# Optimization experiments

Hardware: AMD Instinct MI355X
Metric: run time of the kernel (lower is better)

The kernel has to match this reference:

```python
import jax, jax.numpy as jnp
import numpy as np

B, L, T = 4096, 4096, 2


def setup_inputs() -> dict:
    key = jax.random.key(0)
    k1, k2, k3, k4, k5 = jax.random.split(key, 5)
    emissions = jax.random.normal(k1, (B, L, T), dtype=jnp.float32)
    tags = jax.random.randint(k2, (B, L), 0, T, dtype=jnp.int64)
    mask = jnp.ones((B, L), dtype=jnp.bool_)
    # learned CRF parameters, init uniform(-0.1, 0.1) as in the module
    transitions = jax.random.uniform(k3, (T, T), jnp.float32, -0.1, 0.1)
    start_transitions = jax.random.uniform(k4, (T,), jnp.float32, -0.1, 0.1)
    end_transitions = jax.random.uniform(k5, (T,), jnp.float32, -0.1, 0.1)
    return {"emissions": emissions, "tags": tags, "mask": mask,
            "transitions": transitions, "start_transitions": start_transitions,
            "end_transitions": end_transitions}


def _gold_score(emissions, tags, mask, transitions, start_transitions, end_transitions):
    maskf = mask.astype(emissions.dtype)
    # t=0 contribution
    score = start_transitions[tags[:, 0]] + jnp.take_along_axis(
        emissions[:, 0], tags[:, 0:1], axis=1)[:, 0]
    # steps 1..L-1, fully vectorized
    emit = jnp.take_along_axis(emissions, tags[:, :, None], axis=2)[:, :, 0]  # [B,L]
    trans = transitions[tags[:, 1:], tags[:, :-1]]                            # [B,L-1]
    score = score + jnp.sum((emit[:, 1:] + trans) * maskf[:, 1:], axis=1)
    # end transition from last valid tag
    last_idx = (jnp.sum(mask.astype(jnp.int32), axis=1) - 1)[:, None]         # [B,1]
    last_tags = jnp.take_along_axis(tags, last_idx.astype(tags.dtype), axis=1)[:, 0]
    return score + end_transitions[last_tags]


def _normalizer(emissions, mask, transitions, start_transitions, end_transitions):
    alpha0 = start_transitions + emissions[:, 0]  # [B,T]

    def step(alpha, xm):
        emit, m = xm  # emit: [B,T], m: [B]
        # scores[b, cur, prev] = alpha[b, prev] + transitions[cur, prev]
        scores = alpha[:, None, :] + transitions[None, :, :]
        alpha_new = jax.nn.logsumexp(scores, axis=2) + emit
        alpha = jnp.where(m[:, None], alpha_new, alpha)
        return alpha, None

    emits = jnp.swapaxes(emissions[:, 1:], 0, 1)  # [L-1,B,T]
    masks = jnp.swapaxes(mask[:, 1:], 0, 1)       # [L-1,B]
    alpha, _ = jax.lax.scan(step, alpha0, (emits, masks))
    return jax.nn.logsumexp(alpha + end_transitions, axis=1)  # [B]


def reference(emissions, tags, mask, transitions, start_transitions, end_transitions):
    gold = _gold_score(emissions, tags, mask, transitions, start_transitions, end_transitions)
    fwd = _normalizer(emissions, mask, transitions, start_transitions, end_transitions)
    seq_lengths = jnp.clip(jnp.sum(mask, axis=1).astype(emissions.dtype), 1.0)
    nll = (fwd - gold) / seq_lengths
    return jnp.mean(nll)
```

## Files before the change

kernel.cpp:

```cpp
#include <hip/hip_runtime.h>


typedef float f32x4 __attribute__((ext_vector_type(4)));
typedef int   i32x4 __attribute__((ext_vector_type(4)));

__global__ __launch_bounds__(256, 4) void crf_rows(
    const float* __restrict__ em,
    const int*   __restrict__ tags,
    const float* __restrict__ tr,
    const float* __restrict__ st,
    const float* __restrict__ en,
    float* __restrict__ rows,
    int L)
{
    const int b    = blockIdx.x;
    const int tid  = threadIdx.x;
    const int lane = tid & 63;
    const int wid  = tid >> 6;

    const float t00 = tr[0], t01 = tr[1], t10 = tr[2], t11 = tr[3];
    const float s0 = st[0], s1 = st[1];
    const float en0 = en[0], en1 = en[1];
    const float T00 = __expf(t00), T01 = __expf(t01);
    const float T10 = __expf(t10), T11 = __expf(t11);

    const float* erow = em + (size_t)b * (size_t)(2 * L);
    const int*   trow = tags + (size_t)b * (size_t)L;
    const int l0 = tid << 4;

    f32x4 ev[8];
    const f32x4* ep = reinterpret_cast<const f32x4*>(erow + 2 * l0);
#pragma unroll
    for (int i = 0; i < 8; ++i) ev[i] = ep[i];
    i32x4 tv[4];
    const i32x4* tp = reinterpret_cast<const i32x4*>(trow + l0);
#pragma unroll
    for (int i = 0; i < 2; ++i) tv[i] = tp[i];
    tv[2] = tp[2]; tv[3] = tp[3];
    int pv = trow[tid ? (l0 - 1) : 0];
    asm volatile("" ::
        "v"(ev[0]), "v"(ev[1]), "v"(ev[2]), "v"(ev[3]),
        "v"(ev[4]), "v"(ev[5]), "v"(ev[6]), "v"(ev[7]),
        "v"(tv[0]), "v"(tv[1]), "v"(tv[2]), "v"(tv[3]), "v"(pv));

    const bool is0 = (tid == 0);
    int prev = is0 ? 0 : pv;

    float Q00 = 1.f, Q01 = 0.f, Q10 = 0.f, Q11 = 1.f;
    float ls = 0.f;
    float gold = 0.f;

#pragma unroll
    for (int k = 0; k < 16; ++k) {
        const f32x4 v = ev[k >> 1];
        const float e0 = (k & 1) ? v.z : v.x;
        const float e1 = (k & 1) ? v.w : v.y;
        const i32x4 t4 = tv[k >> 2];
        const int cur = ((k & 3) == 0) ? t4.x : ((k & 3) == 1) ? t4.y
                      : ((k & 3) == 2) ? t4.z : t4.w;

        const float R = __expf(e1 - e0);
        if (!(k == 0 && is0)) {
            const float n00 = fmaf(T00, Q00, T01 * Q10);
            const float n01 = fmaf(T00, Q01, T01 * Q11);
            const float n10 = R * fmaf(T10, Q00, T11 * Q10);
            const float n11 = R * fmaf(T10, Q01, T11 * Q11);
            Q00 = n00; Q01 = n01; Q10 = n10; Q11 = n11;
            ls += e0;
        }

        const float ee  = cur ? e1 : e0;
        const float trv = cur ? (prev ? t11 : t10) : (prev ? t01 : t00);
        if (k == 0 && is0) {
            gold += (cur ? s1 : s0) + ee;
        } else {
            gold += ee + trv;
        }
        prev = cur;
    }
    if (tid == 255) gold += prev ? en1 : en0;

    {
        const float m = fmaxf(fmaxf(Q00, Q01), fmaxf(Q10, Q11));
        const float inv = __builtin_amdgcn_rcpf(m);
        ls += __logf(m);
        Q00 *= inv; Q01 *= inv; Q10 *= inv; Q11 *= inv;
    }
    float sv = ls;

#pragma unroll
    for (int d = 1; d < 64; d <<= 1) {
        const float qb00 = __shfl_down(Q00, d);
        const float qb01 = __shfl_down(Q01, d);
        const float qb10 = __shfl_down(Q10, d);
        const float qb11 = __shfl_down(Q11, d);
        const float sb   = __shfl_down(sv, d);
        const float gb   = __shfl_down(gold, d);
        if (lane + d < 64) {
            const float c00 = fmaf(qb00, Q00, qb01 * Q10);
            const float c01 = fmaf(qb00, Q01, qb01 * Q11);
            const float c10 = fmaf(qb10, Q00, qb11 * Q10);
            const float c11 = fmaf(qb10, Q01, qb11 * Q11);
            Q00 = c00; Q01 = c01; Q10 = c10; Q11 = c11;
            sv += sb; gold += gb;
        }
        if (d == 2 || d == 8 || d == 32) {
            const float m = fmaxf(fmaxf(Q00, Q01), fmaxf(Q10, Q11));
            const float inv = __builtin_amdgcn_rcpf(m);
            sv += __logf(m);
            Q00 *= inv; Q01 *= inv; Q10 *= inv; Q11 *= inv;
        }
    }

    __shared__ float sh[4][6];
    if (lane == 0) {
        sh[wid][0] = sv;  sh[wid][1] = Q00; sh[wid][2] = Q01;
        sh[wid][3] = Q10; sh[wid][4] = Q11; sh[wid][5] = gold;
    }
    __syncthreads();

    if (tid == 0) {
        float S = sh[0][0];
        float A00 = sh[0][1], A01 = sh[0][2], A10 = sh[0][3], A11 = sh[0][4];
        float g = sh[0][5];
#pragma unroll
        for (int w = 1; w < 4; ++w) {
            const float b00 = sh[w][1], b01 = sh[w][2], b10 = sh[w][3], b11 = sh[w][4];
            const float c00 = fmaf(b00, A00, b01 * A10);
            const float c01 = fmaf(b00, A01, b01 * A11);
            const float c10 = fmaf(b10, A00, b11 * A10);
            const float c11 = fmaf(b10, A01, b11 * A11);
            A00 = c00; A01 = c01; A10 = c10; A11 = c11;
            S += sh[w][0]; g += sh[w][5];
        }
        const float a0 = s0 + erow[0];
        const float a1 = s1 + erow[1];
        const float am = fmaxf(a0, a1);
        const float x0 = __expf(a0 - am);
        const float x1 = __expf(a1 - am);
        const float w0 = fmaf(A00, x0, A01 * x1);
        const float w1 = fmaf(A10, x0, A11 * x1);
        const float z  = fmaxf(fmaf(__expf(en0), w0, __expf(en1) * w1), 1e-37f);
        const float fwd = S + am + __logf(z);
        rows[b] = (fwd - g) * (1.0f / (float)L);
    }
}

__global__ __launch_bounds__(256) void reduce_mean(
    const float* __restrict__ rows, float* __restrict__ out, int n)
{
    float s = 0.f;
    for (int i = threadIdx.x; i < n; i += 256) s += rows[i];
#pragma unroll
    for (int sft = 32; sft >= 1; sft >>= 1) s += __shfl_down(s, sft);
    __shared__ float sh[4];
    if ((threadIdx.x & 63) == 0) sh[threadIdx.x >> 6] = s;
    __syncthreads();
    if (threadIdx.x == 0) {
        out[0] = (sh[0] + sh[1] + sh[2] + sh[3]) / (float)n;
    }
}

extern "C" void kernel_launch(void* const* d_in, const int* in_sizes, int n_in,
                              void* d_out, int out_size, void* d_ws, size_t ws_size,
                              hipStream_t stream) {
    const float* em   = (const float*)d_in[0];
    const int*   tags = (const int*)d_in[1];
    const float* tr = (const float*)d_in[3];
    const float* st = (const float*)d_in[4];
    const float* en = (const float*)d_in[5];

    const int B = 4096, L = 4096;
    float* rows = (float*)d_ws;

    crf_rows<<<B, 256, 0, stream>>>(em, tags, tr, st, en, rows, L);
    reduce_mean<<<1, 256, 0, stream>>>(rows, (float*)d_out, B);
}
```

Before: 39.96 us.

## Issue raw asm loads, overlap forward pass with tag loads, count transitions algebraically

Replaces the compiler-generated loads with inline-asm global_load_dwordx4 and uses a partial vmcnt wait, so the forward matrix-product loop runs on emissions while the tag loads are still in flight. The gold score is rebuilt from integer counts of transition types times the four transition values, which removes the per-step selects. Occupancy hint goes from 4 to 6, one renormalisation is dropped from the shuffle tree, and thread 0 reuses register emissions instead of reloading from global memory. The risks are register pressure at the higher occupancy, the fragility of manual waitcnt handling, and wider floating-point range between renormalisations.

```diff
diff --git a/kernel.cpp b/kernel.cpp
--- a/kernel.cpp
+++ b/kernel.cpp
@@ -4,7 +4,7 @@
 typedef float f32x4 __attribute__((ext_vector_type(4)));
 typedef int   i32x4 __attribute__((ext_vector_type(4)));
 
-__global__ __launch_bounds__(256, 4) void crf_rows(
+__global__ __launch_bounds__(256, 6) void crf_rows(
     const float* __restrict__ em,
     const int*   __restrict__ tags,
     const float* __restrict__ tr,
@@ -21,6 +21,9 @@
     const float t00 = tr[0], t01 = tr[1], t10 = tr[2], t11 = tr[3];
     const float s0 = st[0], s1 = st[1];
     const float en0 = en[0], en1 = en[1];
+    asm volatile("" :: "v"(t00), "v"(t01), "v"(t10), "v"(t11),
+                       "v"(s0), "v"(s1), "v"(en0), "v"(en1));
+
     const float T00 = __expf(t00), T01 = __expf(t01);
     const float T10 = __expf(t10), T11 = __expf(t11);
 
@@ -28,28 +31,56 @@
     const int*   trow = tags + (size_t)b * (size_t)L;
     const int l0 = tid << 4;
 
+    unsigned long long ea = (unsigned long long)(erow + 2 * l0);
+    unsigned long long ta = (unsigned long long)(trow + l0);
+    unsigned long long pa = (unsigned long long)(trow + (tid ? (l0 - 1) : 0));
+
     f32x4 ev[8];
-    const f32x4* ep = reinterpret_cast<const f32x4*>(erow + 2 * l0);
-#pragma unroll
-    for (int i = 0; i < 8; ++i) ev[i] = ep[i];
     i32x4 tv[4];
-    const i32x4* tp = reinterpret_cast<const i32x4*>(trow + l0);
-#pragma unroll
-    for (int i = 0; i < 2; ++i) tv[i] = tp[i];
-    tv[2] = tp[2]; tv[3] = tp[3];
-    int pv = trow[tid ? (l0 - 1) : 0];
-    asm volatile("" ::
-        "v"(ev[0]), "v"(ev[1]), "v"(ev[2]), "v"(ev[3]),
-        "v"(ev[4]), "v"(ev[5]), "v"(ev[6]), "v"(ev[7]),
-        "v"(tv[0]), "v"(tv[1]), "v"(tv[2]), "v"(tv[3]), "v"(pv));
+    int pv;
+    asm volatile("global_load_dwordx4 %0, %1, off"            : "=v"(ev[0]) : "v"(ea));
+    asm volatile("global_load_dwordx4 %0, %1, off offset:16"  : "=v"(ev[1]) : "v"(ea));
+    asm volatile("global_load_dwordx4 %0, %1, off offset:32"  : "=v"(ev[2]) : "v"(ea));
+    asm volatile("global_load_dwordx4 %0, %1, off offset:48"  : "=v"(ev[3]) : "v"(ea));
+    asm volatile("global_load_dwordx4 %0, %1, off offset:64"  : "=v"(ev[4]) : "v"(ea));
+    asm volatile("global_load_dwordx4 %0, %1, off offset:80"  : "=v"(ev[5]) : "v"(ea));
+    asm volatile("global_load_dwordx4 %0, %1, off offset:96"  : "=v"(ev[6]) : "v"(ea));
+    asm volatile("global_load_dwordx4 %0, %1, off offset:112" : "=v"(ev[7]) : "v"(ea));
+    asm volatile("global_load_dwordx4 %0, %1, off"            : "=v"(tv[0]) : "v"(ta));
+    asm volatile("global_load_dwordx4 %0, %1, off offset:16"  : "=v"(tv[1]) : "v"(ta));
+    asm volatile("global_load_dwordx4 %0, %1, off offset:32"  : "=v"(tv[2]) : "v"(ta));
+    asm volatile("global_load_dwordx4 %0, %1, off offset:48"  : "=v"(tv[3]) : "v"(ta));
+    asm volatile("global_load_dword   %0, %1, off"            : "=v"(pv)    : "v"(pa));
+
+    asm volatile("s_waitcnt vmcnt(5)" ::: "memory");
+    __builtin_amdgcn_sched_barrier(0);
 
     const bool is0 = (tid == 0);
-    int prev = is0 ? 0 : pv;
 
     float Q00 = 1.f, Q01 = 0.f, Q10 = 0.f, Q11 = 1.f;
     float ls = 0.f;
-    float gold = 0.f;
-
+#pragma unroll
+    for (int k = 0; k < 16; ++k) {
+        const f32x4 v = ev[k >> 1];
+        const float e0 = (k & 1) ? v.z : v.x;
+        const float e1 = (k & 1) ? v.w : v.y;
+        const float R = __expf(e1 - e0);
+        if (!(k == 0 && is0)) {
+            const float m00 = fmaf(T00, Q00, T01 * Q10);
+            const float m01 = fmaf(T00, Q01, T01 * Q11);
+            const float m10 = R * fmaf(T10, Q00, T11 * Q10);
+            const float m11 = R * fmaf(T10, Q01, T11 * Q11);
+            Q00 = m00; Q01 = m01; Q10 = m10; Q11 = m11;
+            ls += e0;
+        }
+    }
+
+    asm volatile("s_waitcnt vmcnt(0)" ::: "memory");
+    __builtin_amdgcn_sched_barrier(0);
+
+    int prev = is0 ? 0 : pv;
+    int itc = 0, ipc = 0;
+    float gd = 0.f;
 #pragma unroll
     for (int k = 0; k < 16; ++k) {
         const f32x4 v = ev[k >> 1];
@@ -58,27 +89,25 @@
         const i32x4 t4 = tv[k >> 2];
         const int cur = ((k & 3) == 0) ? t4.x : ((k & 3) == 1) ? t4.y
                       : ((k & 3) == 2) ? t4.z : t4.w;
-
-        const float R = __expf(e1 - e0);
+        gd += cur ? e1 : e0;
         if (!(k == 0 && is0)) {
-            const float n00 = fmaf(T00, Q00, T01 * Q10);
-            const float n01 = fmaf(T00, Q01, T01 * Q11);
-            const float n10 = R * fmaf(T10, Q00, T11 * Q10);
-            const float n11 = R * fmaf(T10, Q01, T11 * Q11);
-            Q00 = n00; Q01 = n01; Q10 = n10; Q11 = n11;
-            ls += e0;
-        }
-
-        const float ee  = cur ? e1 : e0;
-        const float trv = cur ? (prev ? t11 : t10) : (prev ? t01 : t00);
-        if (k == 0 && is0) {
-            gold += (cur ? s1 : s0) + ee;
-        } else {
-            gold += ee + trv;
+            itc += cur;
+            ipc += prev & cur;
         }
         prev = cur;
     }
-    if (tid == 255) gold += prev ? en1 : en0;
+
+    const int cfirst = tv[0].x;
+    const int clast  = tv[3].w;
+    const int sp  = is0 ? (itc + cfirst - clast) : (pv + itc - clast);
+    const int ntr = is0 ? 15 : 16;
+    float gold = gd
+               + (float)(ntr - itc - sp + ipc) * t00
+               + (float)(sp - ipc)             * t01
+               + (float)(itc - ipc)            * t10
+               + (float)ipc                    * t11;
+    if (is0)        gold += cfirst ? s1 : s0;
+    if (tid == 255) gold += clast ? en1 : en0;
 
     {
         const float m = fmaxf(fmaxf(Q00, Q01), fmaxf(Q10, Q11));
@@ -104,7 +133,7 @@
             Q00 = c00; Q01 = c01; Q10 = c10; Q11 = c11;
             sv += sb; gold += gb;
         }
-        if (d == 2 || d == 8 || d == 32) {
+        if (d == 4 || d == 32) {
             const float m = fmaxf(fmaxf(Q00, Q01), fmaxf(Q10, Q11));
             const float inv = __builtin_amdgcn_rcpf(m);
             sv += __logf(m);
@@ -133,8 +162,8 @@
             A00 = c00; A01 = c01; A10 = c10; A11 = c11;
             S += sh[w][0]; g += sh[w][5];
         }
-        const float a0 = s0 + erow[0];
-        const float a1 = s1 + erow[1];
+        const float a0 = s0 + ev[0].x;
+        const float a1 = s1 + ev[0].y;
         const float am = fmaxf(a0, a1);
         const float x0 = __expf(a0 - am);
         const float x1 = __expf(a1 - am);
```

After: 61.35 us. +53.5%, slower.
